# Performance work log

Hardware: AMD Instinct MI355X
Metric: run time of the kernel (lower is better)

The kernel has to match this reference:

```python
import jax, jax.numpy as jnp
import numpy as np

N_NODES = 100000
N_EDGES = 1600000
DIMS = [128, 128, 40]   # embedding_dim
SS_DIM = 64
DROP_P = 0.2


def setup_inputs() -> dict:
    key = jax.random.key(0)
    ks = jax.random.split(key, 8)
    x = jax.random.normal(ks[0], (N_NODES, DIMS[0]), dtype=jnp.float32)
    adj_row = jax.random.randint(ks[1], (N_EDGES,), 0, N_NODES)
    adj_col = jax.random.randint(ks[2], (N_EDGES,), 0, N_NODES)
    adj_val = jax.random.uniform(ks[3], (N_EDGES,), dtype=jnp.float32)
    # nn.Linear(in, out, bias=False): y = x @ W.T; store transposed as (in, out)
    def lin(k, fi, fo):
        b = 1.0 / np.sqrt(fi)
        return jax.random.uniform(k, (fi, fo), minval=-b, maxval=b, dtype=jnp.float32)
    W0 = lin(ks[4], DIMS[0], DIMS[1])
    W1 = lin(ks[5], DIMS[1], DIMS[2])
    Wss = lin(ks[6], DIMS[-2], SS_DIM)
    return {"x": x, "adj_row": adj_row, "adj_col": adj_col, "adj_val": adj_val,
            "W0": W0, "W1": W1, "Wss": Wss}


def reference(x, adj_row, adj_col, adj_val, W0, W1, Wss):
    N = x.shape[0]
    keep = 1.0 - DROP_P

    def spmm(h):  # sparse [N,N] @ dense [N,d] via gather + segment_sum
        return jax.ops.segment_sum(adj_val[:, None] * h[adj_col], adj_row,
                                   num_segments=N)

    # deterministic dropout masks (fixed key, training path val_test=False)
    k1, k2 = jax.random.split(jax.random.key(42))
    m1 = jax.random.bernoulli(k1, keep, (N, W0.shape[1]))
    m2 = jax.random.bernoulli(k2, keep, (N, W0.shape[1]))

    # main branch: ln=0 -> spmm, lin0, relu, dropout; ln=1 -> spmm, lin1
    h = jnp.where(m1, jax.nn.relu(spmm(x) @ W0) / keep, 0.0)
    h = spmm(h) @ W1

    # self-supervised branch: ln=0 -> spmm, lin0, relu, dropout; ln=1 -> spmm; classifier
    s = jnp.where(m2, jax.nn.relu(spmm(x) @ W0) / keep, 0.0)
    s = spmm(s) @ Wss
    return (h, s)
```

## Files before the change

### kernel.cpp

```cpp
#include <hip/hip_runtime.h>
#include <stdint.h>


#define NN 100000
#define NE 1600000
#define D 128
#define NW 400000
#define ZC 104
#define DO1 40
#define DO2 64
#define OUT_S_OFF 4000000
#define KEEP_THR 6710886u
#define NB 49
#define CAP 36000
#define BINB 196
#define MASKB 3125
#define CSRB 49
#define CONV1K 3125

typedef unsigned int uint;
typedef __attribute__((ext_vector_type(4))) float f32x4;
typedef __attribute__((ext_vector_type(8))) short short8;
union U4S8 { uint4 u; short8 s; };

__device__ __forceinline__ float bflo(uint p) { return __uint_as_float(p << 16); }
__device__ __forceinline__ float bfhi(uint p) { return __uint_as_float(p & 0xffff0000u); }
__device__ __forceinline__ uint f2bf(float f) {
  uint u = __float_as_uint(f);
  return (u + 0x7fffu + ((u >> 16) & 1u)) >> 16;
}
__device__ __forceinline__ uint pack2(float lo, float hi) {
  return f2bf(lo) | (f2bf(hi) << 16);
}

__device__ __forceinline__ void tf2x32(uint k0, uint k1, uint x0, uint x1,
                                       uint& o0, uint& o1) {
  uint ks2 = k0 ^ k1 ^ 0x1BD11BDAu;
  x0 += k0; x1 += k1;
#define TFR(r) { x0 += x1; x1 = (x1 << (r)) | (x1 >> (32 - (r))); x1 ^= x0; }
  TFR(13) TFR(15) TFR(26) TFR(6)
  x0 += k1;  x1 += ks2 + 1u;
  TFR(17) TFR(29) TFR(16) TFR(24)
  x0 += ks2; x1 += k0 + 2u;
  TFR(13) TFR(15) TFR(26) TFR(6)
  x0 += k0;  x1 += k1 + 3u;
  TFR(17) TFR(29) TFR(16) TFR(24)
  x0 += k1;  x1 += ks2 + 4u;
  TFR(13) TFR(15) TFR(26) TFR(6)
  x0 += ks2; x1 += k0 + 5u;
#undef TFR
  o0 = x0; o1 = x1;
}

__global__ void bin_mask_prep_kernel(const int* __restrict__ row, const int* __restrict__ col,
                                     const float* __restrict__ val, int* __restrict__ cursor,
                                     uint2* __restrict__ buck,
                                     uint* __restrict__ m1, uint* __restrict__ m2,
                                     const float* __restrict__ W0, const float* __restrict__ W1,
                                     const float* __restrict__ Wss,
                                     ushort* __restrict__ w0t, ushort* __restrict__ wcatT) {
  int bid = blockIdx.x, tid = threadIdx.x;
  if (bid < BINB) {
    __shared__ int h[NB];
    __shared__ int base[NB];
    if (tid < NB) h[tid] = 0;
    __syncthreads();
    int e0 = bid * 8192;
#pragma unroll 4
    for (int j = 0; j < 32; ++j) {
      int e = e0 + j * 256 + tid;
      if (e < NE) atomicAdd(&h[row[e] >> 11], 1);
    }
    __syncthreads();
    if (tid < NB) {
      int c = h[tid];
      base[tid] = c ? (tid * CAP + atomicAdd(&cursor[tid], c)) : 0;
      h[tid] = 0;
    }
    __syncthreads();
#pragma unroll 4
    for (int j = 0; j < 32; ++j) {
      int e = e0 + j * 256 + tid;
      if (e < NE) {
        int r = row[e];
        int b = r >> 11;
        int k = atomicAdd(&h[b], 1);
        int idx = base[b] + k;
        int lim = (b + 1) * CAP;
        if (idx >= lim) idx = lim - 1;
        buck[idx] = make_uint2(((uint)(r & 2047) << 17) | (uint)col[e],
                               __float_as_uint(val[e]));
      }
    }
  } else if (bid < BINB + MASKB) {
    int t = (bid - BINB) * 256 + tid;
    uint a0, a1, b0, b1;
    tf2x32(0u, 42u, 0u, 0u, a0, a1);
    tf2x32(0u, 42u, 0u, 1u, b0, b1);
    bool second = (t >= NW);
    uint w  = second ? (uint)(t - NW) : (uint)t;
    uint k0 = second ? b0 : a0;
    uint k1 = second ? b1 : a1;
    uint base = w * 32u;
    uint word = 0u;
    for (int i = 0; i < 32; ++i) {
      uint o0, o1;
      tf2x32(k0, k1, 0u, base + (uint)i, o0, o1);
      word |= (uint)(((o0 ^ o1) >> 9) <= KEEP_THR) << i;
    }
    (second ? m2 : m1)[w] = word;
  } else {
    int idx = (bid - BINB - MASKB) * 256 + tid;
    if (idx < 16384) {
      int c = idx >> 7, k = idx & 127;
      w0t[idx] = (ushort)f2bf(W0[k * D + c]);
    } else {
      int j = idx - 16384;
      int c = j >> 7, k = j & 127;
      float v = (c < 40) ? W1[k * DO1 + c] : ((c < 48) ? 0.f : Wss[k * DO2 + (c - 48)]);
      wcatT[j] = (ushort)f2bf(v);
    }
  }
}

__global__ __launch_bounds__(1024) void csr_conv_kernel(
    const uint2* __restrict__ buck, const int* __restrict__ cursor,
    int* __restrict__ ptr, uint2* __restrict__ cv,
    const float* __restrict__ x, uint* __restrict__ xb) {
  int bid = blockIdx.x, tid = threadIdx.x;
  if (bid >= CSRB) {
    int i = (bid - CSRB) * 1024 + tid;
    float4 v = ((const float4*)x)[i];
    ((uint2*)xb)[i] = make_uint2(pack2(v.x, v.y), pack2(v.z, v.w));
    return;
  }
  __shared__ int cnt[2048];
  __shared__ int sc[2048];
  __shared__ int cb[NB];
  int b = bid;
  if (tid < NB) cb[tid] = min(cursor[tid], CAP);
  int i0 = tid, i1 = tid + 1024;
  cnt[i0] = 0; cnt[i1] = 0;
  __syncthreads();
  int gbase = 0;
  for (int i = 0; i < b; ++i) gbase += cb[i];
  int n = cb[b];
  int src = b * CAP;
  for (int i = tid; i < n; i += 1024) atomicAdd(&cnt[buck[src + i].x >> 17], 1);
  __syncthreads();
  sc[i0] = cnt[i0]; sc[i1] = cnt[i1];
  __syncthreads();
  for (int off = 1; off < 2048; off <<= 1) {
    int v0 = (i0 >= off) ? sc[i0 - off] : 0;
    int v1 = (i1 >= off) ? sc[i1 - off] : 0;
    __syncthreads();
    sc[i0] += v0; sc[i1] += v1;
    __syncthreads();
  }
  int r0 = b * 2048;
  int s0 = sc[i0] - cnt[i0], s1 = sc[i1] - cnt[i1];
  if (r0 + i0 < NN) ptr[r0 + i0] = gbase + s0;
  if (r0 + i1 < NN) ptr[r0 + i1] = gbase + s1;
  if (b == 0 && tid == 0) ptr[NN] = NE;
  cnt[i0] = s0; cnt[i1] = s1;
  __syncthreads();
  for (int i = tid; i < n; i += 1024) {
    uint2 e = buck[src + i];
    int rl = e.x >> 17;
    int k = atomicAdd(&cnt[rl], 1);
    cv[gbase + k] = make_uint2(e.x & 0x1FFFFu, e.y);
  }
}

__global__ void spmm_x_kernel(const int* __restrict__ ptr, const uint2* __restrict__ cv,
                              const uint2* __restrict__ xb, uint2* __restrict__ t) {
  int r = blockIdx.x * 8 + (threadIdx.x >> 5);
  int k = threadIdx.x & 31;
  int s = ptr[r], e = ptr[r + 1];
  float a0 = 0.f, a1 = 0.f, a2 = 0.f, a3 = 0.f;
  int i = s;
  for (; i + 8 <= e; i += 8) {
    uint2 ee[8], pp[8];
#pragma unroll
    for (int j = 0; j < 8; ++j) ee[j] = cv[i + j];
#pragma unroll
    for (int j = 0; j < 8; ++j) pp[j] = xb[ee[j].x * 32 + k];
#pragma unroll
    for (int j = 0; j < 8; ++j) {
      float v = __uint_as_float(ee[j].y);
      a0 += v * bflo(pp[j].x); a1 += v * bfhi(pp[j].x);
      a2 += v * bflo(pp[j].y); a3 += v * bfhi(pp[j].y);
    }
  }
  if (i + 4 <= e) {
    uint2 ee[4], pp[4];
#pragma unroll
    for (int j = 0; j < 4; ++j) ee[j] = cv[i + j];
#pragma unroll
    for (int j = 0; j < 4; ++j) pp[j] = xb[ee[j].x * 32 + k];
#pragma unroll
    for (int j = 0; j < 4; ++j) {
      float v = __uint_as_float(ee[j].y);
      a0 += v * bflo(pp[j].x); a1 += v * bfhi(pp[j].x);
      a2 += v * bflo(pp[j].y); a3 += v * bfhi(pp[j].y);
    }
    i += 4;
  }
  for (; i < e; ++i) {
    uint2 ev = cv[i];
    float v = __uint_as_float(ev.y);
    uint2 p = xb[ev.x * 32 + k];
    a0 += v * bflo(p.x); a1 += v * bfhi(p.x);
    a2 += v * bflo(p.y); a3 += v * bfhi(p.y);
  }
  t[r * 32 + k] = make_uint2(pack2(a0, a1), pack2(a2, a3));
}

#define SWZ(row, byte) ((row) * 256 + ((byte) ^ ((((row) >> 1) & 7) << 4)))
__global__ __launch_bounds__(512, 4) void pass_a_kernel(
    const uint* __restrict__ tb, const ushort* __restrict__ w0t,
    const ushort* __restrict__ wcatT,
    const uint* __restrict__ m1, const uint* __restrict__ m2,
    ushort* __restrict__ zz) {
  __shared__ __align__(16) char ldsb[69632];
  uint* mlds = (uint*)(ldsb + 65536);

  int t = threadIdx.x;
  int r0 = blockIdx.x * 128;
  int wid = t >> 6, l = t & 63, lc = l & 15, lk = l >> 4;

#pragma unroll
  for (int i = 0; i < 4; ++i) {
    int lin = i * 512 + t;
    int row = lin >> 4, seg = lin & 15;
    int gr = r0 + row;
    uint4 v = make_uint4(0, 0, 0, 0);
    if (gr < NN) v = ((const uint4*)(tb + (size_t)gr * 64))[seg];
    *(uint4*)&ldsb[SWZ(row, seg * 16)] = v;
    uint4 w = ((const uint4*)w0t)[lin];
    *(uint4*)&ldsb[32768 + SWZ(row, seg * 16)] = w;
  }
#pragma unroll
  for (int i = 0; i < 2; ++i) {
    int idx = t;
    int row = idx >> 2, word = idx & 3;
    int gr = r0 + row;
    uint v = 0;
    if (gr < NN) v = (i == 0 ? m1 : m2)[gr * 4 + word];
    mlds[i * 512 + idx] = v;
  }
  __syncthreads();

  short8 af[4];
#pragma unroll
  for (int s = 0; s < 4; ++s) {
    U4S8 tmp; tmp.u = *(uint4*)&ldsb[SWZ(16 * wid + lc, 64 * s + 16 * lk)];
    af[s] = tmp.s;
  }
  f32x4 acc[8];
#pragma unroll
  for (int n = 0; n < 8; ++n) acc[n] = (f32x4)(0.f);
#pragma unroll
  for (int n = 0; n < 8; ++n) {
#pragma unroll
    for (int s = 0; s < 4; ++s) {
      U4S8 tmp; tmp.u = *(uint4*)&ldsb[32768 + SWZ(16 * n + lc, 64 * s + 16 * lk)];
      acc[n] = __builtin_amdgcn_mfma_f32_16x16x32_bf16(af[s], tmp.s, acc[n], 0, 0, 0);
    }
  }
  __syncthreads();

#pragma unroll
  for (int reg = 0; reg < 4; ++reg) {
    int row = 16 * wid + 4 * lk + reg;
    uint4 w1q = *(uint4*)&mlds[row * 4];
    uint4 w2q = *(uint4*)&mlds[512 + row * 4];
    uint w1a[4] = {w1q.x, w1q.y, w1q.z, w1q.w};
    uint w2a[4] = {w2q.x, w2q.y, w2q.z, w2q.w};
#pragma unroll
    for (int n = 0; n < 8; ++n) {
      float v = fmaxf(acc[n][reg], 0.f) * 1.25f;
      ushort ub = (ushort)f2bf(v);
      int bit = (n & 1) * 16 + lc;
      ushort u1 = ((w1a[n >> 1] >> bit) & 1u) ? ub : (ushort)0;
      ushort u2 = ((w2a[n >> 1] >> bit) & 1u) ? ub : (ushort)0;
      int ad = SWZ(row, 32 * n + 2 * lc);
      *(ushort*)&ldsb[ad] = u1;
      *(ushort*)&ldsb[32768 + ad] = u2;
    }
  }
  __syncthreads();

  f32x4 acc2[7];
#pragma unroll
  for (int n = 0; n < 7; ++n) acc2[n] = (f32x4)(0.f);
#pragma unroll
  for (int n2 = 0; n2 < 7; ++n2) {
    int ubase = (n2 < 3) ? 0 : 32768;
#pragma unroll
    for (int s = 0; s < 4; ++s) {
      U4S8 a2; a2.u = ((const uint4*)wcatT)[(16 * n2 + lc) * 16 + 4 * s + lk];
      U4S8 b2; b2.u = *(uint4*)&ldsb[ubase + SWZ(16 * wid + lc, 64 * s + 16 * lk)];
      acc2[n2] = __builtin_amdgcn_mfma_f32_16x16x32_bf16(a2.s, b2.s, acc2[n2], 0, 0, 0);
    }
  }

  int r = r0 + 16 * wid + lc;
  if (r < NN) {
#pragma unroll
    for (int n2 = 0; n2 < 7; ++n2) {
      if (n2 == 2 && lk >= 2) continue;
      int cb = 16 * n2 + 4 * lk;
      if (n2 >= 3) cb -= 8;
      uint2 v = make_uint2(pack2(acc2[n2][0], acc2[n2][1]),
                           pack2(acc2[n2][2], acc2[n2][3]));
      *(uint2*)(zz + (size_t)r * ZC + cb) = v;
    }
  }
}

__global__ void gather_out_kernel(const int* __restrict__ ptr, const uint2* __restrict__ cv,
                                  const uint2* __restrict__ zp, float* __restrict__ out) {
  int r = blockIdx.x * 8 + (threadIdx.x >> 5);
  int k = threadIdx.x & 31;
  if (k >= 26) return;
  int s = ptr[r], e = ptr[r + 1];
  float a0 = 0.f, a1 = 0.f, a2 = 0.f, a3 = 0.f;
  int i = s;
  for (; i + 8 <= e; i += 8) {
    uint2 ee[8], pp[8];
#pragma unroll
    for (int j = 0; j < 8; ++j) ee[j] = cv[i + j];
#pragma unroll
    for (int j = 0; j < 8; ++j) pp[j] = zp[ee[j].x * 26 + k];
#pragma unroll
    for (int j = 0; j < 8; ++j) {
      float v = __uint_as_float(ee[j].y);
      a0 += v * bflo(pp[j].x); a1 += v * bfhi(pp[j].x);
      a2 += v * bflo(pp[j].y); a3 += v * bfhi(pp[j].y);
    }
  }
  if (i + 4 <= e) {
    uint2 ee[4], pp[4];
#pragma unroll
    for (int j = 0; j < 4; ++j) ee[j] = cv[i + j];
#pragma unroll
    for (int j = 0; j < 4; ++j) pp[j] = zp[ee[j].x * 26 + k];
#pragma unroll
    for (int j = 0; j < 4; ++j) {
      float v = __uint_as_float(ee[j].y);
      a0 += v * bflo(pp[j].x); a1 += v * bfhi(pp[j].x);
      a2 += v * bflo(pp[j].y); a3 += v * bfhi(pp[j].y);
    }
    i += 4;
  }
  for (; i < e; ++i) {
    uint2 ev = cv[i];
    float v = __uint_as_float(ev.y);
    uint2 p = zp[ev.x * 26 + k];
    a0 += v * bflo(p.x); a1 += v * bfhi(p.x);
    a2 += v * bflo(p.y); a3 += v * bfhi(p.y);
  }
  if (k < 10) {
    *(float4*)(out + (size_t)r * DO1 + 4 * k) = make_float4(a0, a1, a2, a3);
  } else {
    *(float4*)(out + OUT_S_OFF + (size_t)r * DO2 + 4 * (k - 10)) = make_float4(a0, a1, a2, a3);
  }
}

extern "C" void kernel_launch(void* const* d_in, const int* in_sizes, int n_in,
                              void* d_out, int out_size, void* d_ws, size_t ws_size,
                              hipStream_t stream) {
  const float* x       = (const float*)d_in[0];
  const int*   adj_row = (const int*)d_in[1];
  const int*   adj_col = (const int*)d_in[2];
  const float* adj_val = (const float*)d_in[3];
  const float* W0      = (const float*)d_in[4];
  const float* W1      = (const float*)d_in[5];
  const float* Wss     = (const float*)d_in[6];
  float* out = (float*)d_out;

  char* ws = (char*)d_ws;
  uint*   t_bf  = (uint*)(ws + 0);
  uint2*  buck  = (uint2*)(ws + 0);
  uint*   xb    = (uint*)(ws + 25600000);
  ushort* zz    = (ushort*)(ws + 25600000);
  uint*   m1    = (uint*)(ws + 51200000);
  uint*   m2    = (uint*)(ws + 52800000);
  int*    ptr   = (int*)(ws + 54400000);
  ushort* w0t   = (ushort*)(ws + 54800016);
  ushort* wcatT = (ushort*)(ws + 54832784);
  int*    curs  = (int*)(ws + 54861456);
  uint2*  cv    = (uint2*)(ws + 55600016);

  hipMemsetAsync(curs, 0, NB * sizeof(int), stream);
  bin_mask_prep_kernel<<<BINB + MASKB + 120, 256, 0, stream>>>(
      adj_row, adj_col, adj_val, curs, buck, m1, m2, W0, W1, Wss, w0t, wcatT);
  csr_conv_kernel<<<CSRB + CONV1K, 1024, 0, stream>>>(buck, curs, ptr, cv, x, xb);
  spmm_x_kernel<<<12500, 256, 0, stream>>>(ptr, cv, (const uint2*)xb, (uint2*)t_bf);
  pass_a_kernel<<<782, 512, 0, stream>>>(t_bf, w0t, wcatT, m1, m2, zz);
  gather_out_kernel<<<12500, 256, 0, stream>>>(ptr, cv, (const uint2*)zz, out);
}
```

Measured before the change: 283.1 us.

## Rebalance pre-pass kernels and pad z rows to 128-element stride

The dropout-mask generation, which is heavy on Threefry arithmetic, moves out of the binning kernel and is interleaved as every fifth block of the memory-bound x SpMM kernel. The x-to-bf16 conversion moves into the binning kernel, so the CSR build now runs as a standalone 49-block kernel. The intent is to hide compute-bound mask work under gather latency and balance the per-kernel load. Separately, the intermediate z buffer row stride grows from 104 to 128 bf16, giving 256-byte-aligned rows for the final gather at the cost of extra write bandwidth and a lower-occupancy CSR launch.

```diff
diff --git a/kernel.cpp b/kernel.cpp
--- a/kernel.cpp
+++ b/kernel.cpp
@@ -6,7 +6,7 @@
 #define NE 1600000
 #define D 128
 #define NW 400000
-#define ZC 104
+#define ZCP 128
 #define DO1 40
 #define DO2 64
 #define OUT_S_OFF 4000000
@@ -14,9 +14,9 @@
 #define NB 49
 #define CAP 36000
 #define BINB 196
+#define CONVB 12500
 #define MASKB 3125
-#define CSRB 49
-#define CONV1K 3125
+#define SPMMB 12500
 
 typedef unsigned int uint;
 typedef __attribute__((ext_vector_type(4))) float f32x4;
@@ -52,10 +52,10 @@
   o0 = x0; o1 = x1;
 }
 
-__global__ void bin_mask_prep_kernel(const int* __restrict__ row, const int* __restrict__ col,
+__global__ void bin_conv_prep_kernel(const int* __restrict__ row, const int* __restrict__ col,
                                      const float* __restrict__ val, int* __restrict__ cursor,
                                      uint2* __restrict__ buck,
-                                     uint* __restrict__ m1, uint* __restrict__ m2,
+                                     const float* __restrict__ x, uint* __restrict__ xb,
                                      const float* __restrict__ W0, const float* __restrict__ W1,
                                      const float* __restrict__ Wss,
                                      ushort* __restrict__ w0t, ushort* __restrict__ wcatT) {
@@ -92,13 +92,77 @@
                                __float_as_uint(val[e]));
       }
     }
-  } else if (bid < BINB + MASKB) {
-    int t = (bid - BINB) * 256 + tid;
+  } else if (bid < BINB + CONVB) {
+    int i = (bid - BINB) * 256 + tid;
+    float4 v = ((const float4*)x)[i];
+    ((uint2*)xb)[i] = make_uint2(pack2(v.x, v.y), pack2(v.z, v.w));
+  } else {
+    int idx = (bid - BINB - CONVB) * 256 + tid;
+    if (idx < 16384) {
+      int c = idx >> 7, k = idx & 127;
+      w0t[idx] = (ushort)f2bf(W0[k * D + c]);
+    } else {
+      int j = idx - 16384;
+      int c = j >> 7, k = j & 127;
+      float v = (c < 40) ? W1[k * DO1 + c] : ((c < 48) ? 0.f : Wss[k * DO2 + (c - 48)]);
+      wcatT[j] = (ushort)f2bf(v);
+    }
+  }
+}
+
+__global__ __launch_bounds__(1024) void csr_kernel(
+    const uint2* __restrict__ buck, const int* __restrict__ cursor,
+    int* __restrict__ ptr, uint2* __restrict__ cv) {
+  __shared__ int cnt[2048];
+  __shared__ int sc[2048];
+  __shared__ int cb[NB];
+  int b = blockIdx.x, tid = threadIdx.x;
+  if (tid < NB) cb[tid] = min(cursor[tid], CAP);
+  int i0 = tid, i1 = tid + 1024;
+  cnt[i0] = 0; cnt[i1] = 0;
+  __syncthreads();
+  int gbase = 0;
+  for (int i = 0; i < b; ++i) gbase += cb[i];
+  int n = cb[b];
+  int src = b * CAP;
+  for (int i = tid; i < n; i += 1024) atomicAdd(&cnt[buck[src + i].x >> 17], 1);
+  __syncthreads();
+  sc[i0] = cnt[i0]; sc[i1] = cnt[i1];
+  __syncthreads();
+  for (int off = 1; off < 2048; off <<= 1) {
+    int v0 = (i0 >= off) ? sc[i0 - off] : 0;
+    int v1 = (i1 >= off) ? sc[i1 - off] : 0;
+    __syncthreads();
+    sc[i0] += v0; sc[i1] += v1;
+    __syncthreads();
+  }
+  int r0 = b * 2048;
+  int s0 = sc[i0] - cnt[i0], s1 = sc[i1] - cnt[i1];
+  if (r0 + i0 < NN) ptr[r0 + i0] = gbase + s0;
+  if (r0 + i1 < NN) ptr[r0 + i1] = gbase + s1;
+  if (b == 0 && tid == 0) ptr[NN] = NE;
+  cnt[i0] = s0; cnt[i1] = s1;
+  __syncthreads();
+  for (int i = tid; i < n; i += 1024) {
+    uint2 e = buck[src + i];
+    int rl = e.x >> 17;
+    int k = atomicAdd(&cnt[rl], 1);
+    cv[gbase + k] = make_uint2(e.x & 0x1FFFFu, e.y);
+  }
+}
+
+__global__ void spmm_mask_kernel(const int* __restrict__ ptr, const uint2* __restrict__ cv,
+                                 const uint2* __restrict__ xb, uint2* __restrict__ t,
+                                 uint* __restrict__ m1, uint* __restrict__ m2) {
+  int bid = blockIdx.x, tid = threadIdx.x;
+  int q = bid / 5, rsel = bid % 5;
+  if (rsel == 4) {
+    int tt = q * 256 + tid;
     uint a0, a1, b0, b1;
     tf2x32(0u, 42u, 0u, 0u, a0, a1);
     tf2x32(0u, 42u, 0u, 1u, b0, b1);
-    bool second = (t >= NW);
-    uint w  = second ? (uint)(t - NW) : (uint)t;
+    bool second = (tt >= NW);
+    uint w  = second ? (uint)(tt - NW) : (uint)tt;
     uint k0 = second ? b0 : a0;
     uint k1 = second ? b1 : a1;
     uint base = w * 32u;
@@ -109,73 +173,11 @@
       word |= (uint)(((o0 ^ o1) >> 9) <= KEEP_THR) << i;
     }
     (second ? m2 : m1)[w] = word;
-  } else {
-    int idx = (bid - BINB - MASKB) * 256 + tid;
-    if (idx < 16384) {
-      int c = idx >> 7, k = idx & 127;
-      w0t[idx] = (ushort)f2bf(W0[k * D + c]);
-    } else {
-      int j = idx - 16384;
-      int c = j >> 7, k = j & 127;
-      float v = (c < 40) ? W1[k * DO1 + c] : ((c < 48) ? 0.f : Wss[k * DO2 + (c - 48)]);
-      wcatT[j] = (ushort)f2bf(v);
-    }
-  }
-}
-
-__global__ __launch_bounds__(1024) void csr_conv_kernel(
-    const uint2* __restrict__ buck, const int* __restrict__ cursor,
-    int* __restrict__ ptr, uint2* __restrict__ cv,
-    const float* __restrict__ x, uint* __restrict__ xb) {
-  int bid = blockIdx.x, tid = threadIdx.x;
-  if (bid >= CSRB) {
-    int i = (bid - CSRB) * 1024 + tid;
-    float4 v = ((const float4*)x)[i];
-    ((uint2*)xb)[i] = make_uint2(pack2(v.x, v.y), pack2(v.z, v.w));
     return;
   }
-  __shared__ int cnt[2048];
-  __shared__ int sc[2048];
-  __shared__ int cb[NB];
-  int b = bid;
-  if (tid < NB) cb[tid] = min(cursor[tid], CAP);
-  int i0 = tid, i1 = tid + 1024;
-  cnt[i0] = 0; cnt[i1] = 0;
-  __syncthreads();
-  int gbase = 0;
-  for (int i = 0; i < b; ++i) gbase += cb[i];
-  int n = cb[b];
-  int src = b * CAP;
-  for (int i = tid; i < n; i += 1024) atomicAdd(&cnt[buck[src + i].x >> 17], 1);
-  __syncthreads();
-  sc[i0] = cnt[i0]; sc[i1] = cnt[i1];
-  __syncthreads();
-  for (int off = 1; off < 2048; off <<= 1) {
-    int v0 = (i0 >= off) ? sc[i0 - off] : 0;
-    int v1 = (i1 >= off) ? sc[i1 - off] : 0;
-    __syncthreads();
-    sc[i0] += v0; sc[i1] += v1;
-    __syncthreads();
-  }
-  int r0 = b * 2048;
-  int s0 = sc[i0] - cnt[i0], s1 = sc[i1] - cnt[i1];
-  if (r0 + i0 < NN) ptr[r0 + i0] = gbase + s0;
-  if (r0 + i1 < NN) ptr[r0 + i1] = gbase + s1;
-  if (b == 0 && tid == 0) ptr[NN] = NE;
-  cnt[i0] = s0; cnt[i1] = s1;
-  __syncthreads();
-  for (int i = tid; i < n; i += 1024) {
-    uint2 e = buck[src + i];
-    int rl = e.x >> 17;
-    int k = atomicAdd(&cnt[rl], 1);
-    cv[gbase + k] = make_uint2(e.x & 0x1FFFFu, e.y);
-  }
-}
-
-__global__ void spmm_x_kernel(const int* __restrict__ ptr, const uint2* __restrict__ cv,
-                              const uint2* __restrict__ xb, uint2* __restrict__ t) {
-  int r = blockIdx.x * 8 + (threadIdx.x >> 5);
-  int k = threadIdx.x & 31;
+  int sb = 4 * q + rsel;
+  int r = sb * 8 + (tid >> 5);
+  int k = tid & 31;
   int s = ptr[r], e = ptr[r + 1];
   float a0 = 0.f, a1 = 0.f, a2 = 0.f, a3 = 0.f;
   int i = s;
@@ -314,7 +316,7 @@
       if (n2 >= 3) cb -= 8;
       uint2 v = make_uint2(pack2(acc2[n2][0], acc2[n2][1]),
                            pack2(acc2[n2][2], acc2[n2][3]));
-      *(uint2*)(zz + (size_t)r * ZC + cb) = v;
+      *(uint2*)(zz + (size_t)r * ZCP + cb) = v;
     }
   }
 }
@@ -332,7 +334,7 @@
 #pragma unroll
     for (int j = 0; j < 8; ++j) ee[j] = cv[i + j];
 #pragma unroll
-    for (int j = 0; j < 8; ++j) pp[j] = zp[ee[j].x * 26 + k];
+    for (int j = 0; j < 8; ++j) pp[j] = zp[ee[j].x * 32 + k];
 #pragma unroll
     for (int j = 0; j < 8; ++j) {
       float v = __uint_as_float(ee[j].y);
@@ -345,7 +347,7 @@
 #pragma unroll
     for (int j = 0; j < 4; ++j) ee[j] = cv[i + j];
 #pragma unroll
-    for (int j = 0; j < 4; ++j) pp[j] = zp[ee[j].x * 26 + k];
+    for (int j = 0; j < 4; ++j) pp[j] = zp[ee[j].x * 32 + k];
 #pragma unroll
     for (int j = 0; j < 4; ++j) {
       float v = __uint_as_float(ee[j].y);
@@ -357,7 +359,7 @@
   for (; i < e; ++i) {
     uint2 ev = cv[i];
     float v = __uint_as_float(ev.y);
-    uint2 p = zp[ev.x * 26 + k];
+    uint2 p = zp[ev.x * 32 + k];
     a0 += v * bflo(p.x); a1 += v * bfhi(p.x);
     a2 += v * bflo(p.y); a3 += v * bfhi(p.y);
   }
@@ -394,10 +396,11 @@
   uint2*  cv    = (uint2*)(ws + 55600016);
 
   hipMemsetAsync(curs, 0, NB * sizeof(int), stream);
-  bin_mask_prep_kernel<<<BINB + MASKB + 120, 256, 0, stream>>>(
-      adj_row, adj_col, adj_val, curs, buck, m1, m2, W0, W1, Wss, w0t, wcatT);
-  csr_conv_kernel<<<CSRB + CONV1K, 1024, 0, stream>>>(buck, curs, ptr, cv, x, xb);
-  spmm_x_kernel<<<12500, 256, 0, stream>>>(ptr, cv, (const uint2*)xb, (uint2*)t_bf);
+  bin_conv_prep_kernel<<<BINB + CONVB + 120, 256, 0, stream>>>(
+      adj_row, adj_col, adj_val, curs, buck, x, xb, W0, W1, Wss, w0t, wcatT);
+  csr_kernel<<<NB, 1024, 0, stream>>>(buck, curs, ptr, cv);
+  spmm_mask_kernel<<<SPMMB + MASKB, 256, 0, stream>>>(ptr, cv, (const uint2*)xb,
+                                                      (uint2*)t_bf, m1, m2);
   pass_a_kernel<<<782, 512, 0, stream>>>(t_bf, w0t, wcatT, m1, m2, zz);
   gather_out_kernel<<<12500, 256, 0, stream>>>(ptr, cv, (const uint2*)zz, out);
 }
```

Result: no change. 281.3 us (-0.6%).
